# Performance work log

Measured on AMD Instinct MI355X. Metric: run time of the kernel, lower is better.

The kernel has to match this reference:

```python
import jax, jax.numpy as jnp
import numpy as np

H = 4096
V = 32000
TEMPERATURE = 1.0
BETA = 0.5


def setup_inputs() -> dict:
    key = jax.random.key(0)
    k1, k2, k3, k4, k5, k6 = jax.random.split(key, 6)
    scale = 1.0 / np.sqrt(H)
    return {
        "student_input": jax.random.normal(k1, (2048, H), dtype=jnp.float32),
        "teacher_input": jax.random.normal(k2, (2048, H), dtype=jnp.float32),
        "W_student": jax.random.uniform(k3, (V, H), dtype=jnp.float32, minval=-scale, maxval=scale),
        "b_student": jax.random.uniform(k4, (V,), dtype=jnp.float32, minval=-scale, maxval=scale),
        "W_teacher": jax.random.uniform(k5, (V, H), dtype=jnp.float32, minval=-scale, maxval=scale),
        "b_teacher": jax.random.uniform(k6, (V,), dtype=jnp.float32, minval=-scale, maxval=scale),
    }


def reference(student_input, teacher_input, W_student, b_student, W_teacher, b_teacher):
    # LM heads: [N, H] @ [H, V] -> [N, V]
    student_logits = jnp.einsum("nh,vh->nv", student_input, W_student) + b_student
    teacher_logits = jnp.einsum("nh,vh->nv", teacher_input, W_teacher) + b_teacher

    log_q = jax.nn.log_softmax(student_logits / TEMPERATURE, axis=-1)  # student
    log_p = jax.nn.log_softmax(teacher_logits / TEMPERATURE, axis=-1)  # teacher

    p = jnp.exp(log_p)
    q = jnp.exp(log_q)
    # mixture m = lerp(q, p, beta) = (1-beta)*q + beta*p
    log_m = jnp.log(BETA * p + (1.0 - BETA) * q)

    # generalized JSD: beta*KL(p||m) + (1-beta)*KL(q||m), batchmean over rows
    per_row = BETA * jnp.sum(p * (log_p - log_m), axis=-1) + (1.0 - BETA) * jnp.sum(
        q * (log_q - log_m), axis=-1
    )
    return jnp.mean(per_row)
```

## Files before the change

### kernel.cpp

```cpp
#include <hip/hip_runtime.h>
#include <hip/hip_bf16.h>

#define NROWS 2048
#define HDIM  4096
#define VDIM  32000

typedef __attribute__((ext_vector_type(8))) __bf16 bf16x8;
typedef __attribute__((ext_vector_type(4))) float floatx4;
typedef __attribute__((ext_vector_type(8))) unsigned short ushort8;

__device__ __forceinline__ unsigned short f2bf(float x) {
  unsigned u = __builtin_bit_cast(unsigned, x);
  return (unsigned short)((u + 0x7fffu + ((u >> 16) & 1u)) >> 16);
}
__device__ __forceinline__ float bf2f(unsigned short h) {
  return __builtin_bit_cast(float, (unsigned)h << 16);
}

__device__ __forceinline__ void ld_lds16(const void* g, void* l) {
  __builtin_amdgcn_global_load_lds(
      (const __attribute__((address_space(1))) void*)g,
      (__attribute__((address_space(3))) void*)l, 16, 0, 0);
}

__global__ __launch_bounds__(256) void cvt_kernel(const float4* __restrict__ in,
                                                  ushort8* __restrict__ out, int n8) {
  for (int i = blockIdx.x * 256 + threadIdx.x; i < n8; i += gridDim.x * 256) {
    float4 v0 = in[2 * i];
    float4 v1 = in[2 * i + 1];
    ushort8 o = {f2bf(v0.x), f2bf(v0.y), f2bf(v0.z), f2bf(v0.w),
                 f2bf(v1.x), f2bf(v1.y), f2bf(v1.z), f2bf(v1.w)};
    out[i] = o;
  }
}

__global__ void zero_out(float* p) { p[0] = 0.0f; }

__global__ __launch_bounds__(256, 2) void gemm_bt(const unsigned short* __restrict__ A,
                                                  const unsigned short* __restrict__ B,
                                                  const float* __restrict__ bias,
                                                  unsigned short* __restrict__ C) {
  __shared__ unsigned short lA[128 * 32];
  __shared__ unsigned short lB[128 * 32];
  const int t = threadIdx.x;
  const int wave = t >> 6;
  const int lane = t & 63;
  const int quad = lane >> 4;
  const int l16 = lane & 15;
  const int waveM = wave & 1;
  const int waveN = wave >> 1;
  const int m0 = blockIdx.x * 128;
  const int v0 = blockIdx.y * 128;

  const int srow = t >> 2;
  const int scolb = (t & 3) * 16;
  const char* gA0 = (const char*)(A + (size_t)(m0 + srow) * HDIM) + scolb;
  const char* gA1 = (const char*)(A + (size_t)(m0 + 64 + srow) * HDIM) + scolb;
  const char* gB0 = (const char*)(B + (size_t)(v0 + srow) * HDIM) + scolb;
  const char* gB1 = (const char*)(B + (size_t)(v0 + 64 + srow) * HDIM) + scolb;
  char* lA0 = (char*)lA + wave * 1024;
  char* lA1 = (char*)lA + 4096 + wave * 1024;
  char* lB0 = (char*)lB + wave * 1024;
  char* lB1 = (char*)lB + 4096 + wave * 1024;

  floatx4 acc[4][4] = {};

  const unsigned short* sAp = lA + (waveM * 64 + l16) * 32 + quad * 8;
  const unsigned short* sBp = lB + (waveN * 64 + l16) * 32 + quad * 8;

  for (int k = 0; k < HDIM; k += 32) {
    const size_t kb = (size_t)k * 2;
    ld_lds16(gA0 + kb, lA0);
    ld_lds16(gA1 + kb, lA1);
    ld_lds16(gB0 + kb, lB0);
    ld_lds16(gB1 + kb, lB1);
    __syncthreads();
    bf16x8 af[4], bfr[4];
#pragma unroll
    for (int i = 0; i < 4; i++) af[i] = *(const bf16x8*)(sAp + i * 16 * 32);
#pragma unroll
    for (int i = 0; i < 4; i++) bfr[i] = *(const bf16x8*)(sBp + i * 16 * 32);
#pragma unroll
    for (int fm = 0; fm < 4; fm++)
#pragma unroll
      for (int fn = 0; fn < 4; fn++)
        acc[fm][fn] =
            __builtin_amdgcn_mfma_f32_16x16x32_bf16(af[fm], bfr[fn], acc[fm][fn], 0, 0, 0);
    __syncthreads();
  }

#pragma unroll
  for (int fn = 0; fn < 4; fn++) {
    const int colv = v0 + waveN * 64 + fn * 16 + l16;
    const float bv = bias[colv];
#pragma unroll
    for (int fm = 0; fm < 4; fm++) {
      const int rbase = m0 + waveM * 64 + fm * 16 + quad * 4;
#pragma unroll
      for (int r = 0; r < 4; r++) {
        C[(size_t)(rbase + r) * VDIM + colv] = f2bf(acc[fm][fn][r] + bv);
      }
    }
  }
}

__global__ __launch_bounds__(256) void stats_jsd(const unsigned short* __restrict__ Ls,
                                                 const unsigned short* __restrict__ Lt,
                                                 float* __restrict__ out) {
  const int row = blockIdx.x;
  const unsigned short* ps = Ls + (size_t)row * VDIM;
  const unsigned short* pt = Lt + (size_t)row * VDIM;
  const int wv = threadIdx.x >> 6;
  __shared__ float red[2][4];
  __shared__ float2 zsh;

  float ms = -1e30f, mt = -1e30f;
  for (int c = threadIdx.x * 8; c < VDIM; c += 2048) {
    ushort8 a = *(const ushort8*)(ps + c);
    ushort8 b = *(const ushort8*)(pt + c);
#pragma unroll
    for (int j = 0; j < 8; j++) {
      ms = fmaxf(ms, bf2f(a[j]));
      mt = fmaxf(mt, bf2f(b[j]));
    }
  }
#pragma unroll
  for (int off = 32; off >= 1; off >>= 1) {
    ms = fmaxf(ms, __shfl_down(ms, off));
    mt = fmaxf(mt, __shfl_down(mt, off));
  }
  if ((threadIdx.x & 63) == 0) { red[0][wv] = ms; red[1][wv] = mt; }
  __syncthreads();
  ms = fmaxf(fmaxf(red[0][0], red[0][1]), fmaxf(red[0][2], red[0][3]));
  mt = fmaxf(fmaxf(red[1][0], red[1][1]), fmaxf(red[1][2], red[1][3]));

  float ss = 0.f, st = 0.f;
  for (int c = threadIdx.x * 8; c < VDIM; c += 2048) {
    ushort8 a = *(const ushort8*)(ps + c);
    ushort8 b = *(const ushort8*)(pt + c);
#pragma unroll
    for (int j = 0; j < 8; j++) {
      ss += __expf(bf2f(a[j]) - ms);
      st += __expf(bf2f(b[j]) - mt);
    }
  }
#pragma unroll
  for (int off = 32; off >= 1; off >>= 1) {
    ss += __shfl_down(ss, off);
    st += __shfl_down(st, off);
  }
  __syncthreads();
  if ((threadIdx.x & 63) == 0) { red[0][wv] = ss; red[1][wv] = st; }
  __syncthreads();
  if (threadIdx.x == 0) {
    zsh = make_float2(ms + __logf(red[0][0] + red[0][1] + red[0][2] + red[0][3]),
                      mt + __logf(red[1][0] + red[1][1] + red[1][2] + red[1][3]));
  }
  __syncthreads();
  const float2 z = zsh;

  float local = 0.f;
  for (int c = threadIdx.x * 8; c < VDIM; c += 2048) {
    ushort8 a = *(const ushort8*)(ps + c);
    ushort8 b = *(const ushort8*)(pt + c);
#pragma unroll
    for (int j = 0; j < 8; j++) {
      float lq = bf2f(a[j]) - z.x;
      float lp = bf2f(b[j]) - z.y;
      float q = __expf(lq);
      float p = __expf(lp);
      float lm = __logf(0.5f * (p + q));
      local += 0.5f * (p * (lp - lm) + q * (lq - lm));
    }
  }
#pragma unroll
  for (int off = 32; off >= 1; off >>= 1) local += __shfl_down(local, off);
  if ((threadIdx.x & 63) == 0) red[0][wv] = local;
  __syncthreads();
  if (threadIdx.x == 0) {
    atomicAdd(out, (red[0][0] + red[0][1] + red[0][2] + red[0][3]) * (1.0f / (float)NROWS));
  }
}

extern "C" void kernel_launch(void* const* d_in, const int* in_sizes, int n_in,
                              void* d_out, int out_size, void* d_ws, size_t ws_size,
                              hipStream_t stream) {
  const float* s_in = (const float*)d_in[0];
  const float* t_in = (const float*)d_in[1];
  const float* W_s = (const float*)d_in[2];
  const float* b_s = (const float*)d_in[3];
  const float* W_t = (const float*)d_in[4];
  const float* b_t = (const float*)d_in[5];
  float* out = (float*)d_out;

  char* ws = (char*)d_ws;
  unsigned short* wsW = (unsigned short*)(ws);
  unsigned short* sA = (unsigned short*)(ws + 262144000);
  unsigned short* tA = (unsigned short*)(ws + 278921216);
  unsigned short* Lsb = (unsigned short*)(ws + 295698432);
  unsigned short* Ltb = (unsigned short*)(ws + 426770432);

  zero_out<<<dim3(1), dim3(1), 0, stream>>>(out);

  cvt_kernel<<<dim3(2048), dim3(256), 0, stream>>>((const float4*)s_in, (ushort8*)sA,
                                                   NROWS * HDIM / 8);
  cvt_kernel<<<dim3(2048), dim3(256), 0, stream>>>((const float4*)t_in, (ushort8*)tA,
                                                   NROWS * HDIM / 8);

  cvt_kernel<<<dim3(2048), dim3(256), 0, stream>>>((const float4*)W_s, (ushort8*)wsW,
                                                   VDIM * HDIM / 8);
  gemm_bt<<<dim3(NROWS / 128, VDIM / 128), dim3(256), 0, stream>>>(sA, wsW, b_s, Lsb);

  cvt_kernel<<<dim3(2048), dim3(256), 0, stream>>>((const float4*)W_t, (ushort8*)wsW,
                                                   VDIM * HDIM / 8);
  gemm_bt<<<dim3(NROWS / 128, VDIM / 128), dim3(256), 0, stream>>>(tA, wsW, b_t, Ltb);

  stats_jsd<<<dim3(NROWS), dim3(256), 0, stream>>>(Lsb, Ltb, out);
}
```

Before: 2.471 ms.

## Replace 128x128 GEMM with 256x256 double-buffered swizzled-LDS MFMA kernel

Replaces the simple single-buffered 128x128 bf16 GEMM with a 512-thread 256x256 tile kernel. It uses 128KB of dynamic LDS with double buffering over K=64 tiles, an XOR-swizzled LDS layout to avoid bank conflicts, and loads staged into LDS in quarters interleaved with MFMA phases under s_setprio. Block IDs are remapped so that workgroups sharing weight tiles are scheduled together. The aim is higher arithmetic intensity and overlap of global loads with compute, at the cost of one block per CU and complex manual waitcnt/barrier logic.

```diff
diff --git a/kernel.cpp b/kernel.cpp
--- a/kernel.cpp
+++ b/kernel.cpp
@@ -4,6 +4,7 @@
 #define NROWS 2048
 #define HDIM  4096
 #define VDIM  32000
+#define KTILES (HDIM / 64)
 
 typedef __attribute__((ext_vector_type(8))) __bf16 bf16x8;
 typedef __attribute__((ext_vector_type(4))) float floatx4;
@@ -22,6 +23,12 @@
       (const __attribute__((address_space(1))) void*)g,
       (__attribute__((address_space(3))) void*)l, 16, 0, 0);
 }
+
+#define MFMA __builtin_amdgcn_mfma_f32_16x16x32_bf16
+#define BAR() __builtin_amdgcn_s_barrier()
+#define WAITL0() asm volatile("s_waitcnt lgkmcnt(0)" ::: "memory")
+#define WAITV6() asm volatile("s_waitcnt vmcnt(6)" ::: "memory")
+#define WAITV0() asm volatile("s_waitcnt vmcnt(0)" ::: "memory")
 
 __global__ __launch_bounds__(256) void cvt_kernel(const float4* __restrict__ in,
                                                   ushort8* __restrict__ out, int n8) {
@@ -36,69 +43,162 @@
 
 __global__ void zero_out(float* p) { p[0] = 0.0f; }
 
-__global__ __launch_bounds__(256, 2) void gemm_bt(const unsigned short* __restrict__ A,
-                                                  const unsigned short* __restrict__ B,
-                                                  const float* __restrict__ bias,
-                                                  unsigned short* __restrict__ C) {
-  __shared__ unsigned short lA[128 * 32];
-  __shared__ unsigned short lB[128 * 32];
+__global__ __launch_bounds__(512, 1) void gemm_bt256(const unsigned short* __restrict__ A,
+                                                     const unsigned short* __restrict__ B,
+                                                     const float* __restrict__ bias,
+                                                     unsigned short* __restrict__ C) {
+  extern __shared__ __align__(16) char smem[];
   const int t = threadIdx.x;
   const int wave = t >> 6;
   const int lane = t & 63;
   const int quad = lane >> 4;
   const int l16 = lane & 15;
-  const int waveM = wave & 1;
-  const int waveN = wave >> 1;
-  const int m0 = blockIdx.x * 128;
-  const int v0 = blockIdx.y * 128;
-
-  const int srow = t >> 2;
-  const int scolb = (t & 3) * 16;
-  const char* gA0 = (const char*)(A + (size_t)(m0 + srow) * HDIM) + scolb;
-  const char* gA1 = (const char*)(A + (size_t)(m0 + 64 + srow) * HDIM) + scolb;
-  const char* gB0 = (const char*)(B + (size_t)(v0 + srow) * HDIM) + scolb;
-  const char* gB1 = (const char*)(B + (size_t)(v0 + 64 + srow) * HDIM) + scolb;
-  char* lA0 = (char*)lA + wave * 1024;
-  char* lA1 = (char*)lA + 4096 + wave * 1024;
-  char* lB0 = (char*)lB + wave * 1024;
-  char* lB1 = (char*)lB + 4096 + wave * 1024;
-
-  floatx4 acc[4][4] = {};
-
-  const unsigned short* sAp = lA + (waveM * 64 + l16) * 32 + quad * 8;
-  const unsigned short* sBp = lB + (waveN * 64 + l16) * 32 + quad * 8;
-
-  for (int k = 0; k < HDIM; k += 32) {
-    const size_t kb = (size_t)k * 2;
-    ld_lds16(gA0 + kb, lA0);
-    ld_lds16(gA1 + kb, lA1);
-    ld_lds16(gB0 + kb, lB0);
-    ld_lds16(gB1 + kb, lB1);
-    __syncthreads();
-    bf16x8 af[4], bfr[4];
-#pragma unroll
-    for (int i = 0; i < 4; i++) af[i] = *(const bf16x8*)(sAp + i * 16 * 32);
-#pragma unroll
-    for (int i = 0; i < 4; i++) bfr[i] = *(const bf16x8*)(sBp + i * 16 * 32);
-#pragma unroll
-    for (int fm = 0; fm < 4; fm++)
-#pragma unroll
-      for (int fn = 0; fn < 4; fn++)
-        acc[fm][fn] =
-            __builtin_amdgcn_mfma_f32_16x16x32_bf16(af[fm], bfr[fn], acc[fm][fn], 0, 0, 0);
-    __syncthreads();
-  }
-
-#pragma unroll
-  for (int fn = 0; fn < 4; fn++) {
-    const int colv = v0 + waveN * 64 + fn * 16 + l16;
+  const int waveN = wave & 3;
+  const int waveM = wave >> 2;
+
+  const int bid = blockIdx.x;
+  const int wgid = (bid & 7) * 125 + (bid >> 3);
+  const int m0 = (wgid & 7) * 256;
+  const int v0 = (wgid >> 3) * 256;
+
+  const int j0r = t >> 3;
+  const int sl = t & 7;
+  const char* pA1[2]; const char* pA2[2]; const char* pB1[2]; const char* pB2[2];
+#pragma unroll
+  for (int j = 0; j < 2; j++) {
+    const int rr = j * 64 + j0r;
+    const int swz = ((sl ^ (rr & 7)) << 4);
+    const int ga1 = (rr & 63) + ((rr >> 6) << 7);
+    const int gb1 = (rr & 31) + ((rr >> 5) << 6);
+    pA1[j] = (const char*)A + (size_t)(m0 + ga1) * (HDIM * 2) + swz;
+    pA2[j] = (const char*)A + (size_t)(m0 + ga1 + 64) * (HDIM * 2) + swz;
+    pB1[j] = (const char*)B + (size_t)(v0 + gb1) * (HDIM * 2) + swz;
+    pB2[j] = (const char*)B + (size_t)(v0 + gb1 + 32) * (HDIM * 2) + swz;
+  }
+  char* ldst = smem + wave * 1024;
+  auto STAGE = [&](char* dst, const char* const* pj, int kt) {
+    ld_lds16(pj[0] + kt * 128, dst);
+    ld_lds16(pj[1] + kt * 128, dst + 8192);
+  };
+
+  const int sx = l16 & 7;
+  const int sk0 = ((0 * 4 + quad) ^ sx) << 4;
+  const int sk1 = ((1 * 4 + quad) ^ sx) << 4;
+  const char* lrdA = smem + (waveM * 64 + l16) * 128;
+  const char* lrdB = smem + 32768 + (waveN * 32 + l16) * 128;
+
+  floatx4 acc[8][4] = {};
+  bf16x8 a[4][2];
+  bf16x8 b0[2][2];
+  bf16x8 b1[2][2];
+
+  STAGE(ldst + 0, pA1, 0);
+  STAGE(ldst + 32768, pB1, 0);
+  STAGE(ldst + 49152, pB2, 0);
+  STAGE(ldst + 16384, pA2, 0);
+  STAGE(ldst + 65536 + 0, pA1, 1);
+  STAGE(ldst + 65536 + 32768, pB1, 1);
+  STAGE(ldst + 65536 + 49152, pB2, 1);
+  WAITV6();
+  BAR();
+
+  auto tileBody = [&](int dOff, int T) {
+    const bool s1 = (T + 1 < KTILES);
+    const bool s2 = (T + 2 < KTILES);
+    const int oOff = 65536 - dOff;
+#pragma unroll
+    for (int m = 0; m < 4; m++) {
+      a[m][0] = *(const bf16x8*)(lrdA + dOff + m * 2048 + sk0);
+      a[m][1] = *(const bf16x8*)(lrdA + dOff + m * 2048 + sk1);
+    }
+#pragma unroll
+    for (int n = 0; n < 2; n++) {
+      b0[n][0] = *(const bf16x8*)(lrdB + dOff + n * 2048 + sk0);
+      b0[n][1] = *(const bf16x8*)(lrdB + dOff + n * 2048 + sk1);
+    }
+    if (s1) STAGE(ldst + oOff + 16384, pA2, T + 1);
+    BAR();
+    WAITL0();
+    __builtin_amdgcn_s_setprio(1);
+#pragma unroll
+    for (int ks = 0; ks < 2; ks++)
+#pragma unroll
+      for (int m = 0; m < 4; m++)
+#pragma unroll
+        for (int n = 0; n < 2; n++)
+          acc[m][n] = MFMA(a[m][ks], b0[n][ks], acc[m][n], 0, 0, 0);
+    __builtin_amdgcn_s_setprio(0);
+    BAR();
+#pragma unroll
+    for (int n = 0; n < 2; n++) {
+      b1[n][0] = *(const bf16x8*)(lrdB + dOff + 16384 + n * 2048 + sk0);
+      b1[n][1] = *(const bf16x8*)(lrdB + dOff + 16384 + n * 2048 + sk1);
+    }
+    if (s2) STAGE(ldst + dOff + 0, pA1, T + 2);
+    BAR();
+    WAITL0();
+    __builtin_amdgcn_s_setprio(1);
+#pragma unroll
+    for (int ks = 0; ks < 2; ks++)
+#pragma unroll
+      for (int m = 0; m < 4; m++)
+#pragma unroll
+        for (int n = 0; n < 2; n++)
+          acc[m][2 + n] = MFMA(a[m][ks], b1[n][ks], acc[m][2 + n], 0, 0, 0);
+    __builtin_amdgcn_s_setprio(0);
+    BAR();
+#pragma unroll
+    for (int m = 0; m < 4; m++) {
+      a[m][0] = *(const bf16x8*)(lrdA + dOff + 16384 + m * 2048 + sk0);
+      a[m][1] = *(const bf16x8*)(lrdA + dOff + 16384 + m * 2048 + sk1);
+    }
+    if (s2) STAGE(ldst + dOff + 32768, pB1, T + 2);
+    BAR();
+    WAITL0();
+    __builtin_amdgcn_s_setprio(1);
+#pragma unroll
+    for (int ks = 0; ks < 2; ks++)
+#pragma unroll
+      for (int m = 0; m < 4; m++)
+#pragma unroll
+        for (int n = 0; n < 2; n++)
+          acc[4 + m][n] = MFMA(a[m][ks], b0[n][ks], acc[4 + m][n], 0, 0, 0);
+    __builtin_amdgcn_s_setprio(0);
+    BAR();
+    if (s2) STAGE(ldst + dOff + 49152, pB2, T + 2);
+    BAR();
+    __builtin_amdgcn_s_setprio(1);
+#pragma unroll
+    for (int ks = 0; ks < 2; ks++)
+#pragma unroll
+      for (int m = 0; m < 4; m++)
+#pragma unroll
+        for (int n = 0; n < 2; n++)
+          acc[4 + m][2 + n] = MFMA(a[m][ks], b1[n][ks], acc[4 + m][2 + n], 0, 0, 0);
+    __builtin_amdgcn_s_setprio(0);
+    if (s2) {
+      WAITV6();
+    } else if (s1) {
+      WAITV0();
+    }
+    BAR();
+  };
+
+  for (int T = 0; T < KTILES; T += 2) {
+    tileBody(0, T);
+    tileBody(65536, T + 1);
+  }
+
+#pragma unroll
+  for (int n = 0; n < 4; n++) {
+    const int colv = v0 + waveN * 64 + n * 16 + l16;
     const float bv = bias[colv];
 #pragma unroll
-    for (int fm = 0; fm < 4; fm++) {
-      const int rbase = m0 + waveM * 64 + fm * 16 + quad * 4;
+    for (int m = 0; m < 8; m++) {
+      const int rbase = m0 + waveM * 128 + m * 16 + quad * 4;
 #pragma unroll
       for (int r = 0; r < 4; r++) {
-        C[(size_t)(rbase + r) * VDIM + colv] = f2bf(acc[fm][fn][r] + bv);
+        C[(size_t)(rbase + r) * VDIM + colv] = f2bf(acc[m][n][r] + bv);
       }
     }
   }
@@ -200,6 +300,13 @@
   unsigned short* Lsb = (unsigned short*)(ws + 295698432);
   unsigned short* Ltb = (unsigned short*)(ws + 426770432);
 
+  static bool lds_opted = false;
+  if (!lds_opted) {
+    (void)hipFuncSetAttribute((const void*)gemm_bt256,
+                              hipFuncAttributeMaxDynamicSharedMemorySize, 131072);
+    lds_opted = true;
+  }
+
   zero_out<<<dim3(1), dim3(1), 0, stream>>>(out);
 
   cvt_kernel<<<dim3(2048), dim3(256), 0, stream>>>((const float4*)s_in, (ushort8*)sA,
@@ -209,11 +316,11 @@
 
   cvt_kernel<<<dim3(2048), dim3(256), 0, stream>>>((const float4*)W_s, (ushort8*)wsW,
                                                    VDIM * HDIM / 8);
-  gemm_bt<<<dim3(NROWS / 128, VDIM / 128), dim3(256), 0, stream>>>(sA, wsW, b_s, Lsb);
+  gemm_bt256<<<dim3(1000), dim3(512), 131072, stream>>>(sA, wsW, b_s, Lsb);
 
   cvt_kernel<<<dim3(2048), dim3(256), 0, stream>>>((const float4*)W_t, (ushort8*)wsW,
                                                    VDIM * HDIM / 8);
-  gemm_bt<<<dim3(NROWS / 128, VDIM / 128), dim3(256), 0, stream>>>(tA, wsW, b_t, Ltb);
+  gemm_bt256<<<dim3(1000), dim3(512), 131072, stream>>>(tA, wsW, b_t, Ltb);
 
   stats_jsd<<<dim3(NROWS), dim3(256), 0, stream>>>(Lsb, Ltb, out);
 }
```

Result: faster. 2.137 ms (-13.5%).
